# Kernel optimization log

Measured on AMD Instinct MI355X. Metric: run time of the kernel, lower is better.

The kernel has to match this reference:

```python
import jax, jax.numpy as jnp
import numpy as np

NODE_DIM = 256
HID = 128        # out_channels per head
HEADS = 4
NLAYERS = 2
OUT_DIM = 128
LM, LT = 30, 50
N = LM + LT       # 80 nodes per duplex graph
F = HID * HEADS   # 512
B = 1024
LN_EPS = 1e-5

def _build_edges():
    off = LM
    ms = np.arange(LM - 1); md = ms + 1
    ts = off + np.arange(LT - 1); td = ts + 1
    s1 = np.concatenate([ms, md, ts, td]); d1 = np.concatenate([md, ms, td, ts])
    ms2 = np.arange(LM - 2); md2 = ms2 + 2
    ts2 = off + np.arange(LT - 2); td2 = ts2 + 2
    s2 = np.concatenate([ms2, md2, ts2, td2]); d2 = np.concatenate([md2, ms2, td2, ts2])
    src = np.concatenate([s1, s2]).astype(np.int32)
    dst = np.concatenate([d1, d2]).astype(np.int32)
    etype = np.concatenate([np.zeros(len(s1), np.int32), np.full(len(s2), 2, np.int32)])
    return src, dst, etype

_SRC0, _DST0, _ETYPE0 = _build_edges()
E0 = len(_SRC0)                      # 308 real edges (backbone + proximity)
SRC = jnp.concatenate([jnp.asarray(_SRC0), jnp.arange(N, dtype=jnp.int32)])  # + self loops
DST = jnp.concatenate([jnp.asarray(_DST0), jnp.arange(N, dtype=jnp.int32)])
DST_BASE = jnp.asarray(_DST0)
ETYPE = jnp.asarray(_ETYPE0)

def _ln(x, g, b):
    mu = x.mean(-1, keepdims=True)
    var = ((x - mu) ** 2).mean(-1, keepdims=True)
    return (x - mu) * jax.lax.rsqrt(var + LN_EPS) * g + b

def setup_inputs() -> dict:
    key = jax.random.key(0)
    ks = jax.random.split(key, 24)
    r = lambda k, shape, fan: jax.random.normal(k, shape, jnp.float32) / np.sqrt(fan)
    inp = {
        'mirna_enc': jax.random.normal(ks[0], (B, LM, NODE_DIM), jnp.float32),
        'target_enc': jax.random.normal(ks[1], (B, LT, NODE_DIM), jnp.float32),
        'node_type_emb': r(ks[2], (2, NODE_DIM), NODE_DIM),
        'edge_type_emb': r(ks[3], (3, HEADS), HEADS),
        'in_W': r(ks[4], (NODE_DIM, F), NODE_DIM), 'in_b': jnp.zeros((F,)),
        'in_ln_g': jnp.ones((F,)), 'in_ln_b': jnp.zeros((F,)),
        'gat_Wl': r(ks[5], (NLAYERS, F, F), F), 'gat_bl': jnp.zeros((NLAYERS, F)),
        'gat_Wr': r(ks[6], (NLAYERS, F, F), F), 'gat_br': jnp.zeros((NLAYERS, F)),
        'gat_We': r(ks[7], (NLAYERS, HEADS, F), HEADS),
        'gat_att': r(ks[8], (NLAYERS, HEADS, HID), HID),
        'gat_bo': jnp.zeros((NLAYERS, F)),
        'ln_g': jnp.ones((NLAYERS, F)), 'ln_b': jnp.zeros((NLAYERS, F)),
        'out_W': r(ks[9], (2 * F, OUT_DIM), 2 * F), 'out_b': jnp.zeros((OUT_DIM,)),
        'out_ln_g': jnp.ones((OUT_DIM,)), 'out_ln_b': jnp.zeros((OUT_DIM,)),
    }
    return inp

def reference(mirna_enc, target_enc, node_type_emb, edge_type_emb, in_W, in_b,
              in_ln_g, in_ln_b, gat_Wl, gat_bl, gat_Wr, gat_br, gat_We, gat_att,
              gat_bo, ln_g, ln_b, out_W, out_b, out_ln_g, out_ln_b):
    bsz = mirna_enc.shape[0]
    x = jnp.concatenate([mirna_enc + node_type_emb[0], target_enc + node_type_emb[1]], axis=1)  # [B,N,256]
    x = jax.nn.gelu(_ln(x @ in_W + in_b, in_ln_g, in_ln_b), approximate=False)  # [B,N,F]
    # edge attributes; self-loop attr = per-dst mean of incoming edge attrs (PyG fill_value='mean')
    base = edge_type_emb[ETYPE]  # [E0, HEADS]
    cnt = jax.ops.segment_sum(jnp.ones((E0, 1), base.dtype), DST_BASE, num_segments=N)
    sl = jax.ops.segment_sum(base, DST_BASE, num_segments=N) / jnp.maximum(cnt, 1.0)
    e_attr = jnp.concatenate([base, sl], axis=0)  # [E, HEADS]
    for i in range(NLAYERS):
        ee = (e_attr @ gat_We[i]).reshape(-1, HEADS, HID)                 # [E,H,C]
        xl = (x @ gat_Wl[i] + gat_bl[i]).reshape(bsz, N, HEADS, HID)
        xr = (x @ gat_Wr[i] + gat_br[i]).reshape(bsz, N, HEADS, HID)
        att_i = gat_att[i]
        def one_graph(xl_b, xr_b):
            msg = xl_b[SRC] + xr_b[DST] + ee                              # [E,H,C]
            a = jnp.einsum('ehc,hc->eh', jax.nn.leaky_relu(msg, 0.2), att_i)
            amax = jax.ops.segment_max(a, DST, num_segments=N)            # every node has a self loop
            ex = jnp.exp(a - amax[DST])
            den = jax.ops.segment_sum(ex, DST, num_segments=N)
            alpha = ex / den[DST]                                         # [E,H]
            out = jax.ops.segment_sum(alpha[:, :, None] * xl_b[SRC], DST, num_segments=N)
            return out.reshape(N, F)
        h = jax.vmap(one_graph)(xl, xr) + gat_bo[i]
        x = _ln(h + x, ln_g[i], ln_b[i])
        if i < NLAYERS - 1:
            x = jax.nn.gelu(x, approximate=False)
    pooled = jnp.concatenate([x.mean(axis=1), x.max(axis=1)], axis=-1)    # [B, 2F]
    return jax.nn.gelu(_ln(pooled @ out_W + out_b, out_ln_g, out_ln_b), approximate=False)
```

## Files before the change

kernel.cpp:

```cpp
#include <hip/hip_runtime.h>
#include <hip/hip_bf16.h>

typedef unsigned short u16;
typedef unsigned int u32;
typedef __attribute__((ext_vector_type(8))) short bf16x8;
typedef __attribute__((ext_vector_type(4))) float f32x4;

#define NB   1024
#define LMI  30
#define LTG  50
#define NN   80
#define ROWS (NB*NN)
#define FF   512
#define HH   4
#define CC   128

__device__ __forceinline__ u16 f2b(float f) {
    u32 u = __float_as_uint(f);
    u32 r = (u + 0x7FFFu + ((u >> 16) & 1u)) >> 16;
    return (u16)r;
}
__device__ __forceinline__ float b2f(u16 h) {
    return __uint_as_float(((u32)h) << 16);
}
__device__ __forceinline__ float gelu_f(float v) {
    return 0.5f * v * (1.0f + erff(v * 0.70710678118654752440f));
}
__device__ __forceinline__ void gload_lds16(const void* g, void* l) {
    __builtin_amdgcn_global_load_lds(
        (__attribute__((address_space(1))) void*)(uintptr_t)g,
        (__attribute__((address_space(3))) void*)(uintptr_t)l,
        16, 0, 0);
}

#define X_OFF     0ULL
#define XLR_OFF   83886080ULL
#define INWT_OFF  251658240ULL
#define WLRT_OFF  (INWT_OFF + 262144ULL)
#define BIAS_OFF  (WLRT_OFF + 2097152ULL)
#define EER_OFF   (BIAS_OFF + 8192ULL)
#define EES_OFF   (EER_OFF + 8192ULL)

__global__ __launch_bounds__(256)
void prep_misc(const float* __restrict__ in_W, const float* __restrict__ gat_Wl,
               const float* __restrict__ gat_bl, const float* __restrict__ gat_Wr,
               const float* __restrict__ gat_br, const float* __restrict__ gat_We,
               const float* __restrict__ eemb,
               u16* __restrict__ inWt, u16* __restrict__ Wlrt,
               float* __restrict__ biaslr, float* __restrict__ eereal,
               float* __restrict__ eeself)
{
    int idx = blockIdx.x * 256 + threadIdx.x;
    if (idx < 131072) {
        int n = idx >> 8, k = idx & 255;
        inWt[idx] = f2b(in_W[k * 512 + n]);
        return;
    }
    idx -= 131072;
    if (idx < 1048576) {
        int l = idx >> 19; int r = idx & 524287; int n = r >> 9, k = r & 511;
        float v = (n < 512) ? gat_Wl[(size_t)l * 262144 + (size_t)k * 512 + n]
                            : gat_Wr[(size_t)l * 262144 + (size_t)k * 512 + (n - 512)];
        Wlrt[idx] = f2b(v);
        return;
    }
    idx -= 1048576;
    if (idx < 2048) {
        int l = idx >> 10, n = idx & 1023;
        biaslr[idx] = (n < 512) ? gat_bl[l * 512 + n] : gat_br[l * 512 + (n - 512)];
        return;
    }
    idx -= 2048;
    if (idx < 2048) {
        int l = idx >> 10; int r = idx & 1023; int t = r >> 9, f = r & 511;
        int et = t ? 2 : 0;
        float v = 0.f;
        #pragma unroll
        for (int h = 0; h < 4; ++h)
            v += eemb[et * 4 + h] * gat_We[l * 2048 + h * 512 + f];
        eereal[idx] = v;
        return;
    }
    idx -= 2048;
    if (idx < 81920) {
        int l = idx / 40960; int r = idx % 40960; int n = r >> 9, f = r & 511;
        int LL = (n < LMI) ? LMI : LTG;
        int p  = (n < LMI) ? n : (n - LMI);
        float c1 = (float)((p >= 1) + (p <= LL - 2));
        float c2 = (float)((p >= 2) + (p <= LL - 3));
        float ic = 1.0f / (c1 + c2);
        float v = 0.f;
        #pragma unroll
        for (int h = 0; h < 4; ++h) {
            float attr = (c1 * eemb[0 * 4 + h] + c2 * eemb[2 * 4 + h]) * ic;
            v += attr * gat_We[l * 2048 + h * 512 + f];
        }
        eeself[idx] = v;
        return;
    }
}

__global__ __launch_bounds__(64)
void prep_xin(const float* __restrict__ mirna, const float* __restrict__ target,
              const float* __restrict__ nte, u16* __restrict__ xin)
{
    int bid = blockIdx.x;
    int b = bid / NN, n = bid % NN;
    int t = threadIdx.x;
    const float* src; const float* tv;
    if (n < LMI) { src = mirna + ((size_t)b * LMI + n) * 256; tv = nte; }
    else         { src = target + ((size_t)b * LTG + (n - LMI)) * 256; tv = nte + 256; }
    float4 v = *(const float4*)(src + t * 4);
    float4 e = *(const float4*)(tv + t * 4);
    u32 p0 = (u32)f2b(v.x + e.x) | ((u32)f2b(v.y + e.y) << 16);
    u32 p1 = (u32)f2b(v.z + e.z) | ((u32)f2b(v.w + e.w) << 16);
    *(uint2*)(xin + (size_t)bid * 256 + t * 4) = make_uint2(p0, p1);
}

template<int N, int K>
__global__ __launch_bounds__(256, 2)
void gemm_nt_bias(const u16* __restrict__ A, const u16* __restrict__ Bt,
                  const float* __restrict__ bias, u16* __restrict__ Cout)
{
    __shared__ __align__(16) u16 sm[2][2][4096];
    const int tid = threadIdx.x;
    const int w = tid >> 6, l = tid & 63;
    constexpr int ncb = N / 128;

    int per = gridDim.x >> 3;
    int nid = (blockIdx.x & 7) * per + (blockIdx.x >> 3);
    const int row0 = (nid / ncb) * 128;
    const int col0 = (nid % ncb) * 128;
    const int wr = (w & 1) * 64, wc = (w >> 1) * 64;

    const int c0 = 2 * w, c1 = 2 * w + 1;
    const int srow = l >> 2;
    const int kperm = (((l & 3) ^ ((l >> 3) & 3))) * 8;
    const u16* Ag0 = A  + (size_t)(row0 + c0 * 16 + srow) * K + kperm;
    const u16* Ag1 = A  + (size_t)(row0 + c1 * 16 + srow) * K + kperm;
    const u16* Bg0 = Bt + (size_t)(col0 + c0 * 16 + srow) * K + kperm;
    const u16* Bg1 = Bt + (size_t)(col0 + c1 * 16 + srow) * K + kperm;

#define STAGE(buf, t) do {                                  \
        int _ko = (t) << 5;                                 \
        gload_lds16(Ag0 + _ko, &sm[buf][0][c0 * 512]);      \
        gload_lds16(Ag1 + _ko, &sm[buf][0][c1 * 512]);      \
        gload_lds16(Bg0 + _ko, &sm[buf][1][c0 * 512]);      \
        gload_lds16(Bg1 + _ko, &sm[buf][1][c1 * 512]);      \
    } while (0)

    f32x4 acc[4][4];
    #pragma unroll
    for (int r = 0; r < 4; ++r)
        #pragma unroll
        for (int f = 0; f < 4; ++f)
            acc[r][f] = (f32x4){0.f, 0.f, 0.f, 0.f};

    constexpr int nsteps = K >> 5;
    STAGE(0, 0);
    __syncthreads();

    const int aoff = (l & 15) * 32 + (((l >> 4) ^ (((l & 15) >> 1) & 3)) * 8);
    const int abase = (wr >> 4) * 512 + aoff;
    const int bbase = (wc >> 4) * 512 + aoff;

    #pragma unroll
    for (int t = 0; t < nsteps; ++t) {
        const int buf = t & 1;
        if (t + 1 < nsteps) STAGE(buf ^ 1, t + 1);
        bf16x8 af[4], bfr[4];
        #pragma unroll
        for (int r = 0; r < 4; ++r)
            af[r] = *(const bf16x8*)&sm[buf][0][abase + r * 512];
        #pragma unroll
        for (int f = 0; f < 4; ++f)
            bfr[f] = *(const bf16x8*)&sm[buf][1][bbase + f * 512];
        #pragma unroll
        for (int r = 0; r < 4; ++r)
            #pragma unroll
            for (int f = 0; f < 4; ++f)
                acc[r][f] = __builtin_amdgcn_mfma_f32_16x16x32_bf16(bfr[f], af[r], acc[r][f], 0, 0, 0);
        __syncthreads();
    }
#undef STAGE

    #pragma unroll
    for (int r = 0; r < 4; ++r) {
        int grow = row0 + wr + r * 16 + (l & 15);
        #pragma unroll
        for (int f = 0; f < 4; ++f) {
            int n0 = col0 + wc + f * 16 + (l >> 4) * 4;
            float4 bv = *(const float4*)(bias + n0);
            u32 lo = (u32)f2b(acc[r][f][0] + bv.x) | ((u32)f2b(acc[r][f][1] + bv.y) << 16);
            u32 hi = (u32)f2b(acc[r][f][2] + bv.z) | ((u32)f2b(acc[r][f][3] + bv.w) << 16);
            *(uint2*)&Cout[(size_t)grow * N + n0] = make_uint2(lo, hi);
        }
    }
}

__global__ __launch_bounds__(256)
void ln_gelu_rows(u16* __restrict__ x, const float* __restrict__ g, const float* __restrict__ b)
{
    int w = threadIdx.x >> 6, l = threadIdx.x & 63;
    size_t row = (size_t)blockIdx.x * 4 + w;
    u16* rp = x + row * FF + l * 8;
    bf16x8 v = *(const bf16x8*)rp;
    float y[8]; float s = 0.f, q = 0.f;
    #pragma unroll
    for (int j = 0; j < 8; ++j) { y[j] = b2f((u16)v[j]); s += y[j]; q += y[j] * y[j]; }
    #pragma unroll
    for (int st = 32; st; st >>= 1) { s += __shfl_xor(s, st, 64); q += __shfl_xor(q, st, 64); }
    float mu = s * (1.0f / 512.0f);
    float var = q * (1.0f / 512.0f) - mu * mu;
    float rs = rsqrtf(var + 1e-5f);
    float4 g0 = *(const float4*)(g + l * 8), g1 = *(const float4*)(g + l * 8 + 4);
    float4 b0 = *(const float4*)(b + l * 8), b1 = *(const float4*)(b + l * 8 + 4);
    float gv[8] = {g0.x, g0.y, g0.z, g0.w, g1.x, g1.y, g1.z, g1.w};
    float bv[8] = {b0.x, b0.y, b0.z, b0.w, b1.x, b1.y, b1.z, b1.w};
    bf16x8 o;
    #pragma unroll
    for (int j = 0; j < 8; ++j) {
        float z = (y[j] - mu) * rs * gv[j] + bv[j];
        o[j] = (short)f2b(gelu_f(z));
    }
    *(bf16x8*)rp = o;
}

__global__ __launch_bounds__(256)
void gat_layer(u16* __restrict__ x, const u16* __restrict__ xlr,
               const float* __restrict__ att, const float* __restrict__ eereal,
               const float* __restrict__ eeself, const float* __restrict__ bo,
               const float* __restrict__ g, const float* __restrict__ bta,
               int apply_gelu)
{
    int tid = threadIdx.x;
    int h = tid >> 6, l = tid & 63;
    int s = l >> 4, t = l & 15;
    int row = blockIdx.x * 4 + s;
    int n = row % NN;
    int lo = (n < LMI) ? 0 : LMI;
    int hi = (n < LMI) ? (LMI - 1) : (NN - 1);
    int c = h * CC + t * 8;

    bf16x8 xrv = *(const bf16x8*)(xlr + (size_t)row * 1024 + 512 + c);
    float xr[8], atv[8];
    #pragma unroll
    for (int j = 0; j < 8; ++j) xr[j] = b2f((u16)xrv[j]);
    {
        float4 a0 = *(const float4*)(att + c), a1 = *(const float4*)(att + c + 4);
        atv[0]=a0.x; atv[1]=a0.y; atv[2]=a0.z; atv[3]=a0.w;
        atv[4]=a1.x; atv[5]=a1.y; atv[6]=a1.z; atv[7]=a1.w;
    }

    bf16x8 vsave[5];
    float p5[5];
    float amax = -1e30f;
    #pragma unroll
    for (int i = 0; i < 5; ++i) {
        int d = i - 2;
        int src = n + d;
        bool ok = (src >= lo) && (src <= hi);
        int dd = ok ? d : 0;
        bf16x8 vv = *(const bf16x8*)(xlr + (size_t)(row + dd) * 1024 + c);
        vsave[i] = vv;
        const float* ee = (i == 2) ? (eeself + (size_t)n * 512 + c)
                        : ((i == 1 || i == 3) ? (eereal + c) : (eereal + 512 + c));
        float4 e0 = *(const float4*)ee, e1 = *(const float4*)(ee + 4);
        float eez[8] = {e0.x, e0.y, e0.z, e0.w, e1.x, e1.y, e1.z, e1.w};
        float p = 0.f;
        #pragma unroll
        for (int j = 0; j < 8; ++j) {
            float m = b2f((u16)vv[j]) + xr[j] + eez[j];
            m = m > 0.f ? m : 0.2f * m;
            p += m * atv[j];
        }
        p += __shfl_xor(p, 1, 64);
        p += __shfl_xor(p, 2, 64);
        p += __shfl_xor(p, 4, 64);
        p += __shfl_xor(p, 8, 64);
        p = ok ? p : -1e30f;
        p5[i] = p;
        amax = fmaxf(amax, p);
    }
    float den = 0.f;
    float o[8] = {0.f,0.f,0.f,0.f,0.f,0.f,0.f,0.f};
    #pragma unroll
    for (int i = 0; i < 5; ++i) {
        float ex = __expf(p5[i] - amax);
        den += ex;
        #pragma unroll
        for (int j = 0; j < 8; ++j) o[j] += ex * b2f((u16)vsave[i][j]);
    }
    float inv = 1.0f / den;

    u16* xrow = x + (size_t)row * FF + c;
    bf16x8 xv = *(const bf16x8*)xrow;
    float bov[8];
    {
        float4 b0 = *(const float4*)(bo + c), b1 = *(const float4*)(bo + c + 4);
        bov[0]=b0.x; bov[1]=b0.y; bov[2]=b0.z; bov[3]=b0.w;
        bov[4]=b1.x; bov[5]=b1.y; bov[6]=b1.z; bov[7]=b1.w;
    }
    float y[8]; float sum = 0.f, sq = 0.f;
    #pragma unroll
    for (int j = 0; j < 8; ++j) {
        y[j] = o[j] * inv + bov[j] + b2f((u16)xv[j]);
        sum += y[j]; sq += y[j] * y[j];
    }
    sum += __shfl_xor(sum, 1, 64); sq += __shfl_xor(sq, 1, 64);
    sum += __shfl_xor(sum, 2, 64); sq += __shfl_xor(sq, 2, 64);
    sum += __shfl_xor(sum, 4, 64); sq += __shfl_xor(sq, 4, 64);
    sum += __shfl_xor(sum, 8, 64); sq += __shfl_xor(sq, 8, 64);

    __shared__ float ssum[4][4], ssq[4][4];
    if (t == 0) { ssum[h][s] = sum; ssq[h][s] = sq; }
    __syncthreads();
    float tot = ssum[0][s] + ssum[1][s] + ssum[2][s] + ssum[3][s];
    float tq  = ssq[0][s] + ssq[1][s] + ssq[2][s] + ssq[3][s];
    float mu = tot * (1.0f / 512.0f);
    float var = tq * (1.0f / 512.0f) - mu * mu;
    float rs = rsqrtf(var + 1e-5f);

    float gv[8], btv[8];
    {
        float4 g0 = *(const float4*)(g + c), g1 = *(const float4*)(g + c + 4);
        float4 t0 = *(const float4*)(bta + c), t1 = *(const float4*)(bta + c + 4);
        gv[0]=g0.x; gv[1]=g0.y; gv[2]=g0.z; gv[3]=g0.w;
        gv[4]=g1.x; gv[5]=g1.y; gv[6]=g1.z; gv[7]=g1.w;
        btv[0]=t0.x; btv[1]=t0.y; btv[2]=t0.z; btv[3]=t0.w;
        btv[4]=t1.x; btv[5]=t1.y; btv[6]=t1.z; btv[7]=t1.w;
    }
    bf16x8 ov;
    #pragma unroll
    for (int j = 0; j < 8; ++j) {
        float z = (y[j] - mu) * rs * gv[j] + btv[j];
        if (apply_gelu) z = gelu_f(z);
        ov[j] = (short)f2b(z);
    }
    *(bf16x8*)xrow = ov;
}

__global__ __launch_bounds__(512)
void pool_kernel(const u16* __restrict__ x, u16* __restrict__ pooled)
{
    int b = blockIdx.x;
    int f = threadIdx.x;
    const u16* base = x + (size_t)b * NN * FF + f;
    float s = 0.f, mx = -1e30f;
    #pragma unroll 4
    for (int n = 0; n < NN; ++n) {
        float v = b2f(base[(size_t)n * FF]);
        s += v; mx = fmaxf(mx, v);
    }
    pooled[(size_t)b * 1024 + f]       = f2b(s * (1.0f / 80.0f));
    pooled[(size_t)b * 1024 + 512 + f] = f2b(mx);
}

__global__ __launch_bounds__(128)
void out_head(const u16* __restrict__ pooled, const float* __restrict__ W,
              const float* __restrict__ bia, const float* __restrict__ g,
              const float* __restrict__ bt, float* __restrict__ out)
{
    int b = blockIdx.x;
    int j = threadIdx.x;
    __shared__ float prow[1024];
    for (int i = j; i < 1024; i += 128) prow[i] = b2f(pooled[(size_t)b * 1024 + i]);
    __syncthreads();
    float acc = 0.f;
    #pragma unroll 8
    for (int k = 0; k < 1024; ++k) acc += prow[k] * W[k * 128 + j];
    acc += bia[j];
    float s = acc, q = acc * acc;
    #pragma unroll
    for (int st = 32; st; st >>= 1) { s += __shfl_xor(s, st, 64); q += __shfl_xor(q, st, 64); }
    __shared__ float ps[2], pq[2];
    int w = j >> 6;
    if ((j & 63) == 0) { ps[w] = s; pq[w] = q; }
    __syncthreads();
    float tot = ps[0] + ps[1], tq = pq[0] + pq[1];
    float mu = tot * (1.0f / 128.0f);
    float var = tq * (1.0f / 128.0f) - mu * mu;
    float rs = rsqrtf(var + 1e-5f);
    float z = (acc - mu) * rs * g[j] + bt[j];
    out[(size_t)b * 128 + j] = gelu_f(z);
}

extern "C" void kernel_launch(void* const* d_in, const int* in_sizes, int n_in,
                              void* d_out, int out_size, void* d_ws, size_t ws_size,
                              hipStream_t stream)
{
    (void)in_sizes; (void)n_in; (void)out_size; (void)ws_size;
    const float* mirna    = (const float*)d_in[0];
    const float* target   = (const float*)d_in[1];
    const float* nte      = (const float*)d_in[2];
    const float* eemb     = (const float*)d_in[3];
    const float* in_W     = (const float*)d_in[4];
    const float* in_b     = (const float*)d_in[5];
    const float* in_ln_g  = (const float*)d_in[6];
    const float* in_ln_b  = (const float*)d_in[7];
    const float* gat_Wl   = (const float*)d_in[8];
    const float* gat_bl   = (const float*)d_in[9];
    const float* gat_Wr   = (const float*)d_in[10];
    const float* gat_br   = (const float*)d_in[11];
    const float* gat_We   = (const float*)d_in[12];
    const float* gat_att  = (const float*)d_in[13];
    const float* gat_bo   = (const float*)d_in[14];
    const float* ln_g     = (const float*)d_in[15];
    const float* ln_b     = (const float*)d_in[16];
    const float* out_W    = (const float*)d_in[17];
    const float* out_b    = (const float*)d_in[18];
    const float* out_ln_g = (const float*)d_in[19];
    const float* out_ln_b = (const float*)d_in[20];

    char* ws = (char*)d_ws;
    u16*   x      = (u16*)(ws + X_OFF);
    u16*   xlr    = (u16*)(ws + XLR_OFF);
    u16*   xin    = xlr;
    u16*   pooled = xlr;
    u16*   inWt   = (u16*)(ws + INWT_OFF);
    u16*   Wlrt   = (u16*)(ws + WLRT_OFF);
    float* biaslr = (float*)(ws + BIAS_OFF);
    float* eereal = (float*)(ws + EER_OFF);
    float* eeself = (float*)(ws + EES_OFF);

    prep_misc<<<4944, 256, 0, stream>>>(in_W, gat_Wl, gat_bl, gat_Wr, gat_br, gat_We, eemb,
                                        inWt, Wlrt, biaslr, eereal, eeself);
    prep_xin<<<ROWS, 64, 0, stream>>>(mirna, target, nte, xin);

    gemm_nt_bias<512, 256><<<(ROWS / 128) * 4, 256, 0, stream>>>(xin, inWt, in_b, x);
    ln_gelu_rows<<<ROWS / 4, 256, 0, stream>>>(x, in_ln_g, in_ln_b);

    for (int l = 0; l < 2; ++l) {
        gemm_nt_bias<1024, 512><<<(ROWS / 128) * 8, 256, 0, stream>>>(
            x, Wlrt + (size_t)l * 524288, biaslr + l * 1024, xlr);
        gat_layer<<<ROWS / 4, 256, 0, stream>>>(x, xlr,
                                                gat_att + l * 512,
                                                eereal + l * 1024,
                                                eeself + (size_t)l * 40960,
                                                gat_bo + l * 512,
                                                ln_g + l * 512, ln_b + l * 512,
                                                (l == 0) ? 1 : 0);
    }

    pool_kernel<<<NB, 512, 0, stream>>>(x, pooled);
    out_head<<<NB, 128, 0, stream>>>(pooled, out_W, out_b, out_ln_g, out_ln_b, (float*)d_out);
}
```

Baseline: 597.8 us.

## Use 256x256 GEMM tiles with 16 waves and a reordered load/compute pipeline

The bf16 NT GEMM moves from 128x128 tiles on 256-thread blocks to 256x256 tiles on 1024-thread blocks, where each of 16 waves computes a 64x64 subtile. This raises operand reuse from LDS and halves global traffic per output. The loop now waits on vmcnt and a barrier at the top, reads its fragments, and only then issues the next stage's prefetch. The MFMA block runs at raised wave priority. The risks are one block per CU, a larger LDS footprint, and a single barrier per step where the prefetch overwrites the buffer other waves may still be reading, a possible race.

```diff
diff --git a/kernel.cpp b/kernel.cpp
--- a/kernel.cpp
+++ b/kernel.cpp
@@ -118,35 +118,30 @@
 }
 
 template<int N, int K>
-__global__ __launch_bounds__(256, 2)
+__global__ __launch_bounds__(1024, 1)
 void gemm_nt_bias(const u16* __restrict__ A, const u16* __restrict__ Bt,
                   const float* __restrict__ bias, u16* __restrict__ Cout)
 {
-    __shared__ __align__(16) u16 sm[2][2][4096];
+    __shared__ __align__(16) u16 sm[2][2][8192];
     const int tid = threadIdx.x;
     const int w = tid >> 6, l = tid & 63;
-    constexpr int ncb = N / 128;
-
-    int per = gridDim.x >> 3;
-    int nid = (blockIdx.x & 7) * per + (blockIdx.x >> 3);
-    const int row0 = (nid / ncb) * 128;
-    const int col0 = (nid % ncb) * 128;
-    const int wr = (w & 1) * 64, wc = (w >> 1) * 64;
-
-    const int c0 = 2 * w, c1 = 2 * w + 1;
+    constexpr int ncb = N / 256;
+    constexpr int nsteps = K >> 5;
+
+    const int per = gridDim.x >> 3;
+    const int nid = (blockIdx.x & 7) * per + (blockIdx.x >> 3);
+    const int row0 = (nid / ncb) * 256;
+    const int col0 = (nid % ncb) * 256;
+    const int wr = w >> 2, wc = w & 3;
+
     const int srow = l >> 2;
-    const int kperm = (((l & 3) ^ ((l >> 3) & 3))) * 8;
-    const u16* Ag0 = A  + (size_t)(row0 + c0 * 16 + srow) * K + kperm;
-    const u16* Ag1 = A  + (size_t)(row0 + c1 * 16 + srow) * K + kperm;
-    const u16* Bg0 = Bt + (size_t)(col0 + c0 * 16 + srow) * K + kperm;
-    const u16* Bg1 = Bt + (size_t)(col0 + c1 * 16 + srow) * K + kperm;
-
-#define STAGE(buf, t) do {                                  \
-        int _ko = (t) << 5;                                 \
-        gload_lds16(Ag0 + _ko, &sm[buf][0][c0 * 512]);      \
-        gload_lds16(Ag1 + _ko, &sm[buf][0][c1 * 512]);      \
-        gload_lds16(Bg0 + _ko, &sm[buf][1][c0 * 512]);      \
-        gload_lds16(Bg1 + _ko, &sm[buf][1][c1 * 512]);      \
+    const int kperm = ((l & 3) ^ ((l >> 3) & 3)) * 8;
+    const u16* Ag = A  + (size_t)(row0 + w * 16 + srow) * K + kperm;
+    const u16* Bg = Bt + (size_t)(col0 + w * 16 + srow) * K + kperm;
+
+#define STAGE(buf, t) do { int _ko = (t) << 5;              \
+        gload_lds16(Ag + _ko, &sm[buf][0][w * 512]);        \
+        gload_lds16(Bg + _ko, &sm[buf][1][w * 512]);        \
     } while (0)
 
     f32x4 acc[4][4];
@@ -156,43 +151,49 @@
         for (int f = 0; f < 4; ++f)
             acc[r][f] = (f32x4){0.f, 0.f, 0.f, 0.f};
 
-    constexpr int nsteps = K >> 5;
     STAGE(0, 0);
-    __syncthreads();
-
-    const int aoff = (l & 15) * 32 + (((l >> 4) ^ (((l & 15) >> 1) & 3)) * 8);
-    const int abase = (wr >> 4) * 512 + aoff;
-    const int bbase = (wc >> 4) * 512 + aoff;
+
+    const int ll = l & 15, lh = l >> 4;
+    const int aoff = ll * 32 + ((lh ^ ((ll >> 1) & 3)) * 8);
+    const int aB = wr * 4 * 512 + aoff;
+    const int bB = wc * 4 * 512 + aoff;
 
     #pragma unroll
     for (int t = 0; t < nsteps; ++t) {
-        const int buf = t & 1;
-        if (t + 1 < nsteps) STAGE(buf ^ 1, t + 1);
+        const int cur = t & 1;
+        asm volatile("s_waitcnt vmcnt(0)" ::: "memory");
+        __builtin_amdgcn_s_barrier();
+
         bf16x8 af[4], bfr[4];
         #pragma unroll
-        for (int r = 0; r < 4; ++r)
-            af[r] = *(const bf16x8*)&sm[buf][0][abase + r * 512];
-        #pragma unroll
-        for (int f = 0; f < 4; ++f)
-            bfr[f] = *(const bf16x8*)&sm[buf][1][bbase + f * 512];
-        #pragma unroll
-        for (int r = 0; r < 4; ++r)
+        for (int ar = 0; ar < 4; ++ar)
+            af[ar] = *(const bf16x8*)&sm[cur][0][aB + ar * 512];
+        #pragma unroll
+        for (int fc = 0; fc < 4; ++fc)
+            bfr[fc] = *(const bf16x8*)&sm[cur][1][bB + fc * 512];
+
+        if (t + 1 < nsteps) STAGE(cur ^ 1, t + 1);
+
+        __builtin_amdgcn_s_setprio(1);
+        #pragma unroll
+        for (int ar = 0; ar < 4; ++ar)
             #pragma unroll
-            for (int f = 0; f < 4; ++f)
-                acc[r][f] = __builtin_amdgcn_mfma_f32_16x16x32_bf16(bfr[f], af[r], acc[r][f], 0, 0, 0);
-        __syncthreads();
+            for (int fc = 0; fc < 4; ++fc)
+                acc[ar][fc] = __builtin_amdgcn_mfma_f32_16x16x32_bf16(
+                    bfr[fc], af[ar], acc[ar][fc], 0, 0, 0);
+        __builtin_amdgcn_s_setprio(0);
     }
 #undef STAGE
 
     #pragma unroll
-    for (int r = 0; r < 4; ++r) {
-        int grow = row0 + wr + r * 16 + (l & 15);
-        #pragma unroll
-        for (int f = 0; f < 4; ++f) {
-            int n0 = col0 + wc + f * 16 + (l >> 4) * 4;
+    for (int ar = 0; ar < 4; ++ar) {
+        int grow = row0 + wr * 64 + ar * 16 + ll;
+        #pragma unroll
+        for (int fc = 0; fc < 4; ++fc) {
+            int n0 = col0 + wc * 64 + fc * 16 + lh * 4;
             float4 bv = *(const float4*)(bias + n0);
-            u32 lo = (u32)f2b(acc[r][f][0] + bv.x) | ((u32)f2b(acc[r][f][1] + bv.y) << 16);
-            u32 hi = (u32)f2b(acc[r][f][2] + bv.z) | ((u32)f2b(acc[r][f][3] + bv.w) << 16);
+            u32 lo = (u32)f2b(acc[ar][fc][0] + bv.x) | ((u32)f2b(acc[ar][fc][1] + bv.y) << 16);
+            u32 hi = (u32)f2b(acc[ar][fc][2] + bv.z) | ((u32)f2b(acc[ar][fc][3] + bv.w) << 16);
             *(uint2*)&Cout[(size_t)grow * N + n0] = make_uint2(lo, hi);
         }
     }
@@ -427,11 +428,11 @@
                                         inWt, Wlrt, biaslr, eereal, eeself);
     prep_xin<<<ROWS, 64, 0, stream>>>(mirna, target, nte, xin);
 
-    gemm_nt_bias<512, 256><<<(ROWS / 128) * 4, 256, 0, stream>>>(xin, inWt, in_b, x);
+    gemm_nt_bias<512, 256><<<(ROWS / 256) * 2, 1024, 0, stream>>>(xin, inWt, in_b, x);
     ln_gelu_rows<<<ROWS / 4, 256, 0, stream>>>(x, in_ln_g, in_ln_b);
 
     for (int l = 0; l < 2; ++l) {
-        gemm_nt_bias<1024, 512><<<(ROWS / 128) * 8, 256, 0, stream>>>(
+        gemm_nt_bias<1024, 512><<<(ROWS / 256) * 4, 1024, 0, stream>>>(
             x, Wlrt + (size_t)l * 524288, biaslr + l * 1024, xlr);
         gat_layer<<<ROWS / 4, 256, 0, stream>>>(x, xlr,
                                                 gat_att + l * 512,
```

After: 567.2 us. -5.1%, faster.
